# Kernel optimization log

Hardware: AMD Instinct MI355X
Metric: run time of the kernel (lower is better)

The kernel has to match this reference:

```python
import jax, jax.numpy as jnp
from jax import lax
import numpy as np

DN = ('NCHW', 'OIHW', 'NCHW')

def conv2d(x, w, b, stride=1, padding=1):
    out = lax.conv_general_dilated(
        x, w, window_strides=(stride, stride),
        padding=[(padding, padding), (padding, padding)],
        dimension_numbers=DN)
    return out + b[None, :, None, None]

def maxpool2d(x, k=2, s=2):
    return lax.reduce_window(x, -jnp.inf, lax.max,
                             window_dimensions=(1, 1, k, k),
                             window_strides=(1, 1, s, s),
                             padding='VALID')

def setup_inputs() -> dict:
    key = jax.random.key(0)
    ks = jax.random.split(key, 9)
    B = 4096
    x = jax.random.normal(ks[0], (B, 3, 32, 32), dtype=jnp.float32)
    # weights initialized like torch.randn(...) * 0.1, biases zeros
    w1 = jax.random.normal(ks[1], (16, 3, 3, 3), dtype=jnp.float32) * 0.1
    b1 = jnp.zeros((16,), jnp.float32)
    w2 = jax.random.normal(ks[2], (32, 16, 3, 3), dtype=jnp.float32) * 0.1
    b2 = jnp.zeros((32,), jnp.float32)
    w3 = jax.random.normal(ks[3], (64, 32, 3, 3), dtype=jnp.float32) * 0.1
    b3 = jnp.zeros((64,), jnp.float32)
    # fc: Linear(64*4*4, 10); kaiming-uniform-ish init
    fan_in = 64 * 4 * 4
    bound = 1.0 / np.sqrt(fan_in)
    fc_w = jax.random.uniform(ks[4], (10, fan_in), jnp.float32, -bound, bound)
    fc_b = jax.random.uniform(ks[5], (10,), jnp.float32, -bound, bound)
    return {"x": x, "w1": w1, "b1": b1, "w2": w2, "b2": b2,
            "w3": w3, "b3": b3, "fc_w": fc_w, "fc_b": fc_b}

def reference(x, w1, b1, w2, b2, w3, b3, fc_w, fc_b):
    h = maxpool2d(jax.nn.relu(conv2d(x, w1, b1)))   # [B,16,16,16]
    h = maxpool2d(jax.nn.relu(conv2d(h, w2, b2)))   # [B,32,8,8]
    h = maxpool2d(jax.nn.relu(conv2d(h, w3, b3)))   # [B,64,4,4]
    h = h.reshape(h.shape[0], -1)                    # [B,1024]
    # dropout is identity in eval mode
    return h @ fc_w.T + fc_b
```

## Files before the change

kernel.cpp:

```cpp
#include <hip/hip_runtime.h>

typedef float f32x4 __attribute__((ext_vector_type(4)));
typedef float f32x16v __attribute__((ext_vector_type(16)));
typedef __bf16 bf16x4 __attribute__((ext_vector_type(4)));
typedef __bf16 bf16x8 __attribute__((ext_vector_type(8)));

union U4B8 { uint4 u; bf16x8 b; };

#define B2P_OFF 0
#define B3P_OFF 9216
#define C1P_OFF 46080

__global__ __launch_bounds__(256) void pack_weights(
    const float* __restrict__ w1, const float* __restrict__ w2,
    const float* __restrict__ w3, __bf16* __restrict__ wsb) {
  int i = blockIdx.x * 256 + threadIdx.x;
  if (i < 9216) {
    int f = i >> 9, r = i & 511;
    int l = r >> 3, j = r & 7;
    int t = f >> 1, p = f & 1;
    int ky = t / 3, kx = t % 3;
    int oc = l & 31, ic = ((l >> 5) << 3) + j;
    float v = w2[oc * 144 + ic * 9 + ky * 3 + kx];
    __bf16 hi = (__bf16)v;
    wsb[B2P_OFF + i] = p ? (__bf16)(v - (float)hi) : hi;
  } else if (i < 9216 + 36864) {
    int q = i - 9216;
    int f = q >> 9, r = q & 511;
    int l = r >> 3, j = r & 7;
    int t = f >> 3, nt = (f >> 1) & 3, p = f & 1;
    int ky = t / 3, kx = t % 3;
    int oc = nt * 16 + (l & 15), ic = ((l >> 4) << 3) + j;
    float v = w3[oc * 288 + ic * 9 + ky * 3 + kx];
    __bf16 hi = (__bf16)v;
    wsb[B3P_OFF + q] = p ? (__bf16)(v - (float)hi) : hi;
  } else if (i < 9216 + 36864 + 1024) {
    int q = i - (9216 + 36864);
    int f = q >> 9, r = q & 511;
    int l = r >> 3, j = r & 7;
    int oc = l & 15, kg = l >> 4;
    int half = j >> 2, ic = j & 3;
    float v = 0.f;
    if (ic < 3) {
      if (f == 0) {
        if (kg < 3)            v = w1[oc * 27 + ic * 9 + kg * 3 + half];
        else if (half == 0)    v = w1[oc * 27 + ic * 9 + 0 * 3 + 2];
      } else {
        if (half == 0 && kg < 2) v = w1[oc * 27 + ic * 9 + (kg + 1) * 3 + 2];
      }
    }
    wsb[C1P_OFF + q] = (__bf16)v;
  }
}

__global__ __launch_bounds__(256, 4) void cnn_fused(
    const float* __restrict__ x, const __bf16* __restrict__ wsb,
    const float* __restrict__ b1, const float* __restrict__ b2,
    const float* __restrict__ b3,
    const float* __restrict__ fcw, const float* __restrict__ fcb,
    float* __restrict__ out) {
  __shared__ __align__(16) unsigned char smem[25408];
  __bf16* s_img = (__bf16*)smem;
  __bf16* s2b   = (__bf16*)(smem + 9280);
  __bf16* s3b   = (__bf16*)smem;
  float*  h3s   = (float*)(smem + 9280);

  const __bf16* b2p = wsb + B2P_OFF;
  const __bf16* b3p = wsb + B3P_OFF;
  const __bf16* c1p = wsb + C1P_OFF;

  const int tid = threadIdx.x;
  const int img = blockIdx.x;
  const int w = tid >> 6, lane = tid & 63;

  if (tid < 132) {
    int row, col;
    if (tid < 34)       { row = 0;        col = tid; }
    else if (tid < 68)  { row = 33;       col = tid - 34; }
    else if (tid < 100) { row = tid - 67; col = 0; }
    else                { row = tid - 99; col = 33; }
    *(unsigned long long*)&s_img[(row * 34 + col) * 4] = 0ull;
  } else if (tid >= 248 && tid < 252) {
    *(unsigned long long*)&s_img[4624 + (tid - 248) * 4] = 0ull;
  }
  {
    const float* xg = x + img * 3072;
    const int r = tid * 4;
    const int y = r >> 5, xx = r & 31;
    const f32x4 c0 = *(const f32x4*)&xg[r];
    const f32x4 c1 = *(const f32x4*)&xg[r + 1024];
    const f32x4 c2 = *(const f32x4*)&xg[r + 2048];
    #pragma unroll
    for (int k = 0; k < 4; ++k) {
      bf16x4 pk;
      pk.x = (__bf16)c0[k];
      pk.y = (__bf16)c1[k];
      pk.z = (__bf16)c2[k];
      pk.w = (__bf16)0.f;
      *(bf16x4*)&s_img[((y + 1) * 34 + (xx + k + 1)) * 4] = pk;
    }
  }
  const bf16x8 B1h = *(const bf16x8*)(c1p + lane * 8);
  const bf16x8 B2h = *(const bf16x8*)(c1p + 512 + lane * 8);
  __syncthreads();

  float pooled[16];
  {
    const int xm = lane & 15, kg = lane >> 4;
    const int d1r = (kg == 3) ? 0 : kg;
    const int d1c = (kg == 3) ? 2 : 0;
    const int d2r = (kg == 0) ? 1 : 2;
    const int dd1 = d1r * 34 + d1c;
    const int dd2 = d2r * 34 + 2;
    #pragma unroll
    for (int p = 0; p < 4; ++p) {
      f32x4 acc[2][2];
      #pragma unroll
      for (int ys = 0; ys < 2; ++ys)
        #pragma unroll
        for (int xh = 0; xh < 2; ++xh)
          #pragma unroll
          for (int r = 0; r < 4; ++r) acc[ys][xh][r] = 0.f;
      #pragma unroll
      for (int ys = 0; ys < 2; ++ys) {
        const int yqg = w * 8 + p * 2 + ys;
        #pragma unroll
        for (int xh = 0; xh < 2; ++xh) {
          const int cb = yqg * 34 + xh * 16 + xm;
          const uint2 p0 = *(const uint2*)&s_img[(cb + dd1) * 4];
          const uint2 p1 = *(const uint2*)&s_img[(cb + dd1 + 1) * 4];
          const uint2 p2 = *(const uint2*)&s_img[(cb + dd2) * 4];
          const uint2 p3 = *(const uint2*)&s_img[(cb + dd2 + 1) * 4];
          U4B8 A1, A2;
          A1.u.x = p0.x; A1.u.y = p0.y; A1.u.z = p1.x; A1.u.w = p1.y;
          A2.u.x = p2.x; A2.u.y = p2.y; A2.u.z = p3.x; A2.u.w = p3.y;
          acc[ys][xh] = __builtin_amdgcn_mfma_f32_16x16x32_bf16(A1.b, B1h, acc[ys][xh], 0, 0, 0);
          acc[ys][xh] = __builtin_amdgcn_mfma_f32_16x16x32_bf16(A2.b, B2h, acc[ys][xh], 0, 0, 0);
        }
      }
      #pragma unroll
      for (int xh = 0; xh < 2; ++xh)
        #pragma unroll
        for (int xp2 = 0; xp2 < 2; ++xp2) {
          const float v0 = fmaxf(acc[0][xh][xp2 * 2], acc[0][xh][xp2 * 2 + 1]);
          const float v1 = fmaxf(acc[1][xh][xp2 * 2], acc[1][xh][xp2 * 2 + 1]);
          pooled[p * 4 + xh * 2 + xp2] = fmaxf(v0, v1);
        }
    }
  }

  if (tid < 68) {
    int row, col;
    if (tid < 18)      { row = 0;       col = tid; }
    else if (tid < 36) { row = 17;      col = tid - 18; }
    else if (tid < 52) { row = tid - 35; col = 0; }
    else               { row = tid - 51; col = 17; }
    unsigned long long* p = (unsigned long long*)&s2b[row * 448 + col * 24];
    p[0] = 0ull; p[1] = 0ull; p[2] = 0ull; p[3] = 0ull;
  }
  {
    const int oc = lane & 15, quad = lane >> 4;
    const float bias = b1[oc];
    #pragma unroll
    for (int p = 0; p < 4; ++p)
      #pragma unroll
      for (int xh = 0; xh < 2; ++xh)
        #pragma unroll
        for (int xp2 = 0; xp2 < 2; ++xp2) {
          const float v = fmaxf(pooled[p * 4 + xh * 2 + xp2] + bias, 0.f);
          const int py = w * 4 + p, px = xh * 8 + quad * 2 + xp2;
          s2b[(py + 1) * 448 + (px + 1) * 24 + oc] = (__bf16)v;
        }
  }
  bf16x8 Bf[9];
  #pragma unroll
  for (int t = 0; t < 9; ++t)
    Bf[t] = *(const bf16x8*)(b2p + (t * 2) * 512 + lane * 8);
  __syncthreads();

  float pooled2[8];
  {
    const unsigned short* s2 = (const unsigned short*)s2b;
    const int xm = lane & 15, yoff = (lane >> 4) & 1, kh = lane >> 5;
    #pragma unroll
    for (int i2 = 0; i2 < 2; ++i2) {
      f32x16v acc;
      #pragma unroll
      for (int r = 0; r < 16; ++r) acc[r] = 0.f;
      const int rbase = (4 * w + yoff + 2 * i2) * 448;
      #pragma unroll
      for (int t = 0; t < 9; ++t) {
        const int ky = t / 3, kx = t % 3;
        const int ro = rbase + ky * 448 + (xm + kx) * 24 + kh * 8;
        bf16x8 ah = *(const bf16x8*)&s2[ro];
        acc = __builtin_amdgcn_mfma_f32_32x32x16_bf16(ah, Bf[t], acc, 0, 0, 0);
      }
      #pragma unroll
      for (int bq = 0; bq < 2; ++bq)
        #pragma unroll
        for (int rq = 0; rq < 2; ++rq) {
          const int r0 = bq * 4 + rq * 2;
          pooled2[i2 * 4 + bq * 2 + rq] =
              fmaxf(fmaxf(acc[r0], acc[r0 + 1]), fmaxf(acc[r0 + 8], acc[r0 + 9]));
        }
    }
  }

  if (tid < 36) {
    int row, col;
    if (tid < 10)      { row = 0;       col = tid; }
    else if (tid < 20) { row = 9;       col = tid - 10; }
    else if (tid < 28) { row = tid - 19; col = 0; }
    else               { row = tid - 27; col = 9; }
    unsigned long long* p = (unsigned long long*)&s3b[row * 448 + col * 40];
    #pragma unroll
    for (int u = 0; u < 8; ++u) p[u] = 0ull;
  }
  {
    const int oc = lane & 31, hh = lane >> 5;
    const float bias = b2[oc];
    #pragma unroll
    for (int i2 = 0; i2 < 2; ++i2)
      #pragma unroll
      for (int bq = 0; bq < 2; ++bq)
        #pragma unroll
        for (int rq = 0; rq < 2; ++rq) {
          const float v = fmaxf(pooled2[i2 * 4 + bq * 2 + rq] + bias, 0.f);
          const int py = 2 * w + i2, px = 2 * hh + 4 * bq + rq;
          s3b[(py + 1) * 448 + (px + 1) * 40 + oc] = (__bf16)v;
        }
  }
  __syncthreads();

  {
    const unsigned short* s3 = (const unsigned short*)s3b;
    const int nt = w;
    bf16x8 Bt[9];
    #pragma unroll
    for (int t = 0; t < 9; ++t)
      Bt[t] = *(const bf16x8*)(b3p + (t * 8 + nt * 2) * 512 + lane * 8);
    const int m = lane & 15, quad = lane >> 4;
    const int xm = m & 7, yoff = m >> 3;
    f32x4 acc[4];
    #pragma unroll
    for (int mt = 0; mt < 4; ++mt)
      #pragma unroll
      for (int r = 0; r < 4; ++r) acc[mt][r] = 0.f;
    #pragma unroll
    for (int t = 0; t < 9; ++t) {
      const int ky = t / 3, kx = t % 3;
      #pragma unroll
      for (int mt = 0; mt < 4; ++mt) {
        const int ro = (2 * mt + yoff + ky) * 448 + (xm + kx) * 40 + quad * 8;
        bf16x8 ah = *(const bf16x8*)&s3[ro];
        acc[mt] = __builtin_amdgcn_mfma_f32_16x16x32_bf16(ah, Bt[t], acc[mt], 0, 0, 0);
      }
    }
    const int ocl = lane & 15;
    #pragma unroll
    for (int mt = 0; mt < 4; ++mt) {
      float p0 = fmaxf(acc[mt][0], acc[mt][1]);
      float p1 = fmaxf(acc[mt][2], acc[mt][3]);
      p0 = fmaxf(p0, __shfl_xor(p0, 32, 64));
      p1 = fmaxf(p1, __shfl_xor(p1, 32, 64));
      if (quad < 2) {
        const int oc = nt * 16 + ocl;
        const float bias = b3[oc];
        const int base = oc * 20 + mt * 4 + (quad & 1) * 2;
        h3s[base]     = fmaxf(p0 + bias, 0.f);
        h3s[base + 1] = fmaxf(p1 + bias, 0.f);
      }
    }
  }
  __syncthreads();

  {
    f32x4 hv[4];
    #pragma unroll
    for (int k = 0; k < 4; ++k) hv[k] = *(const f32x4*)&h3s[lane * 20 + k * 4];
    for (int j = w; j < 10; j += 4) {
      const f32x4* fw4 = (const f32x4*)&fcw[j * 1024 + lane * 16];
      float dot = 0.f;
      #pragma unroll
      for (int k = 0; k < 4; ++k) {
        const f32x4 fv = fw4[k];
        dot = fmaf(hv[k][0], fv[0], dot);
        dot = fmaf(hv[k][1], fv[1], dot);
        dot = fmaf(hv[k][2], fv[2], dot);
        dot = fmaf(hv[k][3], fv[3], dot);
      }
      #pragma unroll
      for (int s = 32; s > 0; s >>= 1) dot += __shfl_xor(dot, s, 64);
      if (lane == 0) out[img * 10 + j] = dot + fcb[j];
    }
  }
}

extern "C" void kernel_launch(void* const* d_in, const int* in_sizes, int n_in,
                              void* d_out, int out_size, void* d_ws, size_t ws_size,
                              hipStream_t stream) {
  const float* x   = (const float*)d_in[0];
  const float* w1  = (const float*)d_in[1];
  const float* b1  = (const float*)d_in[2];
  const float* w2  = (const float*)d_in[3];
  const float* b2  = (const float*)d_in[4];
  const float* w3  = (const float*)d_in[5];
  const float* b3  = (const float*)d_in[6];
  const float* fcw = (const float*)d_in[7];
  const float* fcb = (const float*)d_in[8];
  __bf16* wsb = (__bf16*)d_ws;
  float* out = (float*)d_out;

  hipLaunchKernelGGL(pack_weights, dim3(184), dim3(256), 0, stream, w1, w2, w3, wsb);
  hipLaunchKernelGGL(cnn_fused, dim3(4096), dim3(256), 0, stream,
                     x, wsb, b1, b2, b3, fcw, fcb, out);
}
```

Measured before the change: 125.3 us.

## Process two images per workgroup to amortize weight loads and interleave MFMAs

Each 256-thread block now handles two images instead of one, with doubled shared memory (two image buffers) and half the grid. Weight fragments loaded into registers for each conv stage and the FC weights are reused across both images, and independent MFMA chains for the two images are interleaved to hide latency. In exchange register pressure and LDS use double, and the occupancy hint drops from 4 to 3 blocks per CU.

```diff
diff --git a/kernel.cpp b/kernel.cpp
--- a/kernel.cpp
+++ b/kernel.cpp
@@ -53,58 +53,63 @@
   }
 }
 
-__global__ __launch_bounds__(256, 4) void cnn_fused(
+__global__ __launch_bounds__(256, 3) void cnn_fused(
     const float* __restrict__ x, const __bf16* __restrict__ wsb,
     const float* __restrict__ b1, const float* __restrict__ b2,
     const float* __restrict__ b3,
     const float* __restrict__ fcw, const float* __restrict__ fcb,
     float* __restrict__ out) {
-  __shared__ __align__(16) unsigned char smem[25408];
-  __bf16* s_img = (__bf16*)smem;
-  __bf16* s2b   = (__bf16*)(smem + 9280);
-  __bf16* s3b   = (__bf16*)smem;
-  float*  h3s   = (float*)(smem + 9280);
+  __shared__ __align__(16) unsigned char smem[50816];
 
   const __bf16* b2p = wsb + B2P_OFF;
   const __bf16* b3p = wsb + B3P_OFF;
   const __bf16* c1p = wsb + C1P_OFF;
 
   const int tid = threadIdx.x;
-  const int img = blockIdx.x;
   const int w = tid >> 6, lane = tid & 63;
-
-  if (tid < 132) {
-    int row, col;
-    if (tid < 34)       { row = 0;        col = tid; }
-    else if (tid < 68)  { row = 33;       col = tid - 34; }
-    else if (tid < 100) { row = tid - 67; col = 0; }
-    else                { row = tid - 99; col = 33; }
-    *(unsigned long long*)&s_img[(row * 34 + col) * 4] = 0ull;
-  } else if (tid >= 248 && tid < 252) {
-    *(unsigned long long*)&s_img[4624 + (tid - 248) * 4] = 0ull;
-  }
-  {
-    const float* xg = x + img * 3072;
+  const int img0 = blockIdx.x * 2;
+
+  #pragma unroll
+  for (int im = 0; im < 2; ++im) {
+    __bf16* s_img = (__bf16*)(smem + im * 25408);
+    if (tid < 132) {
+      int row, col;
+      if (tid < 34)       { row = 0;        col = tid; }
+      else if (tid < 68)  { row = 33;       col = tid - 34; }
+      else if (tid < 100) { row = tid - 67; col = 0; }
+      else                { row = tid - 99; col = 33; }
+      *(unsigned long long*)&s_img[(row * 34 + col) * 4] = 0ull;
+    } else if (tid >= 248 && tid < 252) {
+      *(unsigned long long*)&s_img[4624 + (tid - 248) * 4] = 0ull;
+    }
+  }
+  {
     const int r = tid * 4;
     const int y = r >> 5, xx = r & 31;
-    const f32x4 c0 = *(const f32x4*)&xg[r];
-    const f32x4 c1 = *(const f32x4*)&xg[r + 1024];
-    const f32x4 c2 = *(const f32x4*)&xg[r + 2048];
+    const float* xg0 = x + img0 * 3072;
+    const float* xg1 = xg0 + 3072;
+    const f32x4 a0 = *(const f32x4*)&xg0[r];
+    const f32x4 a1 = *(const f32x4*)&xg0[r + 1024];
+    const f32x4 a2 = *(const f32x4*)&xg0[r + 2048];
+    const f32x4 d0 = *(const f32x4*)&xg1[r];
+    const f32x4 d1 = *(const f32x4*)&xg1[r + 1024];
+    const f32x4 d2 = *(const f32x4*)&xg1[r + 2048];
+    __bf16* si0 = (__bf16*)smem;
+    __bf16* si1 = (__bf16*)(smem + 25408);
     #pragma unroll
     for (int k = 0; k < 4; ++k) {
-      bf16x4 pk;
-      pk.x = (__bf16)c0[k];
-      pk.y = (__bf16)c1[k];
-      pk.z = (__bf16)c2[k];
-      pk.w = (__bf16)0.f;
-      *(bf16x4*)&s_img[((y + 1) * 34 + (xx + k + 1)) * 4] = pk;
+      bf16x4 pa, pb;
+      pa.x = (__bf16)a0[k]; pa.y = (__bf16)a1[k]; pa.z = (__bf16)a2[k]; pa.w = (__bf16)0.f;
+      pb.x = (__bf16)d0[k]; pb.y = (__bf16)d1[k]; pb.z = (__bf16)d2[k]; pb.w = (__bf16)0.f;
+      *(bf16x4*)&si0[((y + 1) * 34 + (xx + k + 1)) * 4] = pa;
+      *(bf16x4*)&si1[((y + 1) * 34 + (xx + k + 1)) * 4] = pb;
     }
   }
   const bf16x8 B1h = *(const bf16x8*)(c1p + lane * 8);
   const bf16x8 B2h = *(const bf16x8*)(c1p + 512 + lane * 8);
   __syncthreads();
 
-  float pooled[16];
+  float pooled[2][16];
   {
     const int xm = lane & 15, kg = lane >> 4;
     const int d1r = (kg == 3) ? 0 : kg;
@@ -114,63 +119,79 @@
     const int dd2 = d2r * 34 + 2;
     #pragma unroll
     for (int p = 0; p < 4; ++p) {
-      f32x4 acc[2][2];
-      #pragma unroll
-      for (int ys = 0; ys < 2; ++ys)
-        #pragma unroll
-        for (int xh = 0; xh < 2; ++xh)
-          #pragma unroll
-          for (int r = 0; r < 4; ++r) acc[ys][xh][r] = 0.f;
+      f32x4 acc[2][2][2];
+      #pragma unroll
+      for (int im = 0; im < 2; ++im)
+        #pragma unroll
+        for (int ys = 0; ys < 2; ++ys)
+          #pragma unroll
+          for (int xh = 0; xh < 2; ++xh)
+            #pragma unroll
+            for (int r = 0; r < 4; ++r) acc[im][ys][xh][r] = 0.f;
       #pragma unroll
       for (int ys = 0; ys < 2; ++ys) {
         const int yqg = w * 8 + p * 2 + ys;
         #pragma unroll
         for (int xh = 0; xh < 2; ++xh) {
           const int cb = yqg * 34 + xh * 16 + xm;
-          const uint2 p0 = *(const uint2*)&s_img[(cb + dd1) * 4];
-          const uint2 p1 = *(const uint2*)&s_img[(cb + dd1 + 1) * 4];
-          const uint2 p2 = *(const uint2*)&s_img[(cb + dd2) * 4];
-          const uint2 p3 = *(const uint2*)&s_img[(cb + dd2 + 1) * 4];
-          U4B8 A1, A2;
-          A1.u.x = p0.x; A1.u.y = p0.y; A1.u.z = p1.x; A1.u.w = p1.y;
-          A2.u.x = p2.x; A2.u.y = p2.y; A2.u.z = p3.x; A2.u.w = p3.y;
-          acc[ys][xh] = __builtin_amdgcn_mfma_f32_16x16x32_bf16(A1.b, B1h, acc[ys][xh], 0, 0, 0);
-          acc[ys][xh] = __builtin_amdgcn_mfma_f32_16x16x32_bf16(A2.b, B2h, acc[ys][xh], 0, 0, 0);
+          #pragma unroll
+          for (int im = 0; im < 2; ++im) {
+            const __bf16* si = (const __bf16*)(smem + im * 25408);
+            const uint2 p0 = *(const uint2*)&si[(cb + dd1) * 4];
+            const uint2 p1 = *(const uint2*)&si[(cb + dd1 + 1) * 4];
+            const uint2 p2 = *(const uint2*)&si[(cb + dd2) * 4];
+            const uint2 p3 = *(const uint2*)&si[(cb + dd2 + 1) * 4];
+            U4B8 A1, A2;
+            A1.u.x = p0.x; A1.u.y = p0.y; A1.u.z = p1.x; A1.u.w = p1.y;
+            A2.u.x = p2.x; A2.u.y = p2.y; A2.u.z = p3.x; A2.u.w = p3.y;
+            acc[im][ys][xh] = __builtin_amdgcn_mfma_f32_16x16x32_bf16(A1.b, B1h, acc[im][ys][xh], 0, 0, 0);
+            acc[im][ys][xh] = __builtin_amdgcn_mfma_f32_16x16x32_bf16(A2.b, B2h, acc[im][ys][xh], 0, 0, 0);
+          }
         }
       }
       #pragma unroll
-      for (int xh = 0; xh < 2; ++xh)
-        #pragma unroll
-        for (int xp2 = 0; xp2 < 2; ++xp2) {
-          const float v0 = fmaxf(acc[0][xh][xp2 * 2], acc[0][xh][xp2 * 2 + 1]);
-          const float v1 = fmaxf(acc[1][xh][xp2 * 2], acc[1][xh][xp2 * 2 + 1]);
-          pooled[p * 4 + xh * 2 + xp2] = fmaxf(v0, v1);
-        }
-    }
-  }
-
-  if (tid < 68) {
-    int row, col;
-    if (tid < 18)      { row = 0;       col = tid; }
-    else if (tid < 36) { row = 17;      col = tid - 18; }
-    else if (tid < 52) { row = tid - 35; col = 0; }
-    else               { row = tid - 51; col = 17; }
-    unsigned long long* p = (unsigned long long*)&s2b[row * 448 + col * 24];
-    p[0] = 0ull; p[1] = 0ull; p[2] = 0ull; p[3] = 0ull;
+      for (int im = 0; im < 2; ++im)
+        #pragma unroll
+        for (int xh = 0; xh < 2; ++xh)
+          #pragma unroll
+          for (int xp2 = 0; xp2 < 2; ++xp2) {
+            const float v0 = fmaxf(acc[im][0][xh][xp2 * 2], acc[im][0][xh][xp2 * 2 + 1]);
+            const float v1 = fmaxf(acc[im][1][xh][xp2 * 2], acc[im][1][xh][xp2 * 2 + 1]);
+            pooled[im][p * 4 + xh * 2 + xp2] = fmaxf(v0, v1);
+          }
+    }
+  }
+
+  #pragma unroll
+  for (int im = 0; im < 2; ++im) {
+    __bf16* s2b = (__bf16*)(smem + im * 25408 + 9280);
+    if (tid < 68) {
+      int row, col;
+      if (tid < 18)      { row = 0;       col = tid; }
+      else if (tid < 36) { row = 17;      col = tid - 18; }
+      else if (tid < 52) { row = tid - 35; col = 0; }
+      else               { row = tid - 51; col = 17; }
+      unsigned long long* p = (unsigned long long*)&s2b[row * 448 + col * 24];
+      p[0] = 0ull; p[1] = 0ull; p[2] = 0ull; p[3] = 0ull;
+    }
   }
   {
     const int oc = lane & 15, quad = lane >> 4;
     const float bias = b1[oc];
     #pragma unroll
-    for (int p = 0; p < 4; ++p)
-      #pragma unroll
-      for (int xh = 0; xh < 2; ++xh)
-        #pragma unroll
-        for (int xp2 = 0; xp2 < 2; ++xp2) {
-          const float v = fmaxf(pooled[p * 4 + xh * 2 + xp2] + bias, 0.f);
-          const int py = w * 4 + p, px = xh * 8 + quad * 2 + xp2;
-          s2b[(py + 1) * 448 + (px + 1) * 24 + oc] = (__bf16)v;
-        }
+    for (int im = 0; im < 2; ++im) {
+      __bf16* s2b = (__bf16*)(smem + im * 25408 + 9280);
+      #pragma unroll
+      for (int p = 0; p < 4; ++p)
+        #pragma unroll
+        for (int xh = 0; xh < 2; ++xh)
+          #pragma unroll
+          for (int xp2 = 0; xp2 < 2; ++xp2) {
+            const float v = fmaxf(pooled[im][p * 4 + xh * 2 + xp2] + bias, 0.f);
+            const int py = w * 4 + p, px = xh * 8 + quad * 2 + xp2;
+            s2b[(py + 1) * 448 + (px + 1) * 24 + oc] = (__bf16)v;
+          }
+    }
   }
   bf16x8 Bf[9];
   #pragma unroll
@@ -178,62 +199,76 @@
     Bf[t] = *(const bf16x8*)(b2p + (t * 2) * 512 + lane * 8);
   __syncthreads();
 
-  float pooled2[8];
-  {
-    const unsigned short* s2 = (const unsigned short*)s2b;
+  float pooled2[2][8];
+  {
+    const unsigned short* s2_0 = (const unsigned short*)(smem + 9280);
+    const unsigned short* s2_1 = (const unsigned short*)(smem + 25408 + 9280);
     const int xm = lane & 15, yoff = (lane >> 4) & 1, kh = lane >> 5;
     #pragma unroll
     for (int i2 = 0; i2 < 2; ++i2) {
-      f32x16v acc;
-      #pragma unroll
-      for (int r = 0; r < 16; ++r) acc[r] = 0.f;
+      f32x16v accA, accB;
+      #pragma unroll
+      for (int r = 0; r < 16; ++r) { accA[r] = 0.f; accB[r] = 0.f; }
       const int rbase = (4 * w + yoff + 2 * i2) * 448;
       #pragma unroll
       for (int t = 0; t < 9; ++t) {
         const int ky = t / 3, kx = t % 3;
         const int ro = rbase + ky * 448 + (xm + kx) * 24 + kh * 8;
-        bf16x8 ah = *(const bf16x8*)&s2[ro];
-        acc = __builtin_amdgcn_mfma_f32_32x32x16_bf16(ah, Bf[t], acc, 0, 0, 0);
+        bf16x8 a0 = *(const bf16x8*)&s2_0[ro];
+        bf16x8 a1 = *(const bf16x8*)&s2_1[ro];
+        accA = __builtin_amdgcn_mfma_f32_32x32x16_bf16(a0, Bf[t], accA, 0, 0, 0);
+        accB = __builtin_amdgcn_mfma_f32_32x32x16_bf16(a1, Bf[t], accB, 0, 0, 0);
       }
       #pragma unroll
       for (int bq = 0; bq < 2; ++bq)
         #pragma unroll
         for (int rq = 0; rq < 2; ++rq) {
           const int r0 = bq * 4 + rq * 2;
-          pooled2[i2 * 4 + bq * 2 + rq] =
-              fmaxf(fmaxf(acc[r0], acc[r0 + 1]), fmaxf(acc[r0 + 8], acc[r0 + 9]));
+          pooled2[0][i2 * 4 + bq * 2 + rq] =
+              fmaxf(fmaxf(accA[r0], accA[r0 + 1]), fmaxf(accA[r0 + 8], accA[r0 + 9]));
+          pooled2[1][i2 * 4 + bq * 2 + rq] =
+              fmaxf(fmaxf(accB[r0], accB[r0 + 1]), fmaxf(accB[r0 + 8], accB[r0 + 9]));
         }
     }
   }
 
-  if (tid < 36) {
-    int row, col;
-    if (tid < 10)      { row = 0;       col = tid; }
-    else if (tid < 20) { row = 9;       col = tid - 10; }
-    else if (tid < 28) { row = tid - 19; col = 0; }
-    else               { row = tid - 27; col = 9; }
-    unsigned long long* p = (unsigned long long*)&s3b[row * 448 + col * 40];
-    #pragma unroll
-    for (int u = 0; u < 8; ++u) p[u] = 0ull;
+  #pragma unroll
+  for (int im = 0; im < 2; ++im) {
+    __bf16* s3b = (__bf16*)(smem + im * 25408);
+    if (tid < 36) {
+      int row, col;
+      if (tid < 10)      { row = 0;       col = tid; }
+      else if (tid < 20) { row = 9;       col = tid - 10; }
+      else if (tid < 28) { row = tid - 19; col = 0; }
+      else               { row = tid - 27; col = 9; }
+      unsigned long long* p = (unsigned long long*)&s3b[row * 448 + col * 40];
+      #pragma unroll
+      for (int u = 0; u < 8; ++u) p[u] = 0ull;
+    }
   }
   {
     const int oc = lane & 31, hh = lane >> 5;
     const float bias = b2[oc];
     #pragma unroll
-    for (int i2 = 0; i2 < 2; ++i2)
-      #pragma unroll
-      for (int bq = 0; bq < 2; ++bq)
-        #pragma unroll
-        for (int rq = 0; rq < 2; ++rq) {
-          const float v = fmaxf(pooled2[i2 * 4 + bq * 2 + rq] + bias, 0.f);
-          const int py = 2 * w + i2, px = 2 * hh + 4 * bq + rq;
-          s3b[(py + 1) * 448 + (px + 1) * 40 + oc] = (__bf16)v;
-        }
+    for (int im = 0; im < 2; ++im) {
+      __bf16* s3b = (__bf16*)(smem + im * 25408);
+      #pragma unroll
+      for (int i2 = 0; i2 < 2; ++i2)
+        #pragma unroll
+        for (int bq = 0; bq < 2; ++bq)
+          #pragma unroll
+          for (int rq = 0; rq < 2; ++rq) {
+            const float v = fmaxf(pooled2[im][i2 * 4 + bq * 2 + rq] + bias, 0.f);
+            const int py = 2 * w + i2, px = 2 * hh + 4 * bq + rq;
+            s3b[(py + 1) * 448 + (px + 1) * 40 + oc] = (__bf16)v;
+          }
+    }
   }
   __syncthreads();
 
   {
-    const unsigned short* s3 = (const unsigned short*)s3b;
+    const unsigned short* s3_0 = (const unsigned short*)smem;
+    const unsigned short* s3_1 = (const unsigned short*)(smem + 25408);
     const int nt = w;
     bf16x8 Bt[9];
     #pragma unroll
@@ -241,57 +276,80 @@
       Bt[t] = *(const bf16x8*)(b3p + (t * 8 + nt * 2) * 512 + lane * 8);
     const int m = lane & 15, quad = lane >> 4;
     const int xm = m & 7, yoff = m >> 3;
-    f32x4 acc[4];
-    #pragma unroll
-    for (int mt = 0; mt < 4; ++mt)
-      #pragma unroll
-      for (int r = 0; r < 4; ++r) acc[mt][r] = 0.f;
+    f32x4 acc[2][4];
+    #pragma unroll
+    for (int im = 0; im < 2; ++im)
+      #pragma unroll
+      for (int mt = 0; mt < 4; ++mt)
+        #pragma unroll
+        for (int r = 0; r < 4; ++r) acc[im][mt][r] = 0.f;
     #pragma unroll
     for (int t = 0; t < 9; ++t) {
       const int ky = t / 3, kx = t % 3;
       #pragma unroll
       for (int mt = 0; mt < 4; ++mt) {
         const int ro = (2 * mt + yoff + ky) * 448 + (xm + kx) * 40 + quad * 8;
-        bf16x8 ah = *(const bf16x8*)&s3[ro];
-        acc[mt] = __builtin_amdgcn_mfma_f32_16x16x32_bf16(ah, Bt[t], acc[mt], 0, 0, 0);
+        bf16x8 a0 = *(const bf16x8*)&s3_0[ro];
+        bf16x8 a1 = *(const bf16x8*)&s3_1[ro];
+        acc[0][mt] = __builtin_amdgcn_mfma_f32_16x16x32_bf16(a0, Bt[t], acc[0][mt], 0, 0, 0);
+        acc[1][mt] = __builtin_amdgcn_mfma_f32_16x16x32_bf16(a1, Bt[t], acc[1][mt], 0, 0, 0);
       }
     }
     const int ocl = lane & 15;
     #pragma unroll
-    for (int mt = 0; mt < 4; ++mt) {
-      float p0 = fmaxf(acc[mt][0], acc[mt][1]);
-      float p1 = fmaxf(acc[mt][2], acc[mt][3]);
-      p0 = fmaxf(p0, __shfl_xor(p0, 32, 64));
-      p1 = fmaxf(p1, __shfl_xor(p1, 32, 64));
-      if (quad < 2) {
-        const int oc = nt * 16 + ocl;
-        const float bias = b3[oc];
-        const int base = oc * 20 + mt * 4 + (quad & 1) * 2;
-        h3s[base]     = fmaxf(p0 + bias, 0.f);
-        h3s[base + 1] = fmaxf(p1 + bias, 0.f);
+    for (int im = 0; im < 2; ++im) {
+      float* h3s = (float*)(smem + im * 25408 + 9280);
+      #pragma unroll
+      for (int mt = 0; mt < 4; ++mt) {
+        float p0 = fmaxf(acc[im][mt][0], acc[im][mt][1]);
+        float p1 = fmaxf(acc[im][mt][2], acc[im][mt][3]);
+        p0 = fmaxf(p0, __shfl_xor(p0, 32, 64));
+        p1 = fmaxf(p1, __shfl_xor(p1, 32, 64));
+        if (quad < 2) {
+          const int oc = nt * 16 + ocl;
+          const float bias = b3[oc];
+          const int base = oc * 20 + mt * 4 + (quad & 1) * 2;
+          h3s[base]     = fmaxf(p0 + bias, 0.f);
+          h3s[base + 1] = fmaxf(p1 + bias, 0.f);
+        }
       }
     }
   }
   __syncthreads();
 
   {
-    f32x4 hv[4];
-    #pragma unroll
-    for (int k = 0; k < 4; ++k) hv[k] = *(const f32x4*)&h3s[lane * 20 + k * 4];
+    const float* h3s0 = (const float*)(smem + 9280);
+    const float* h3s1 = (const float*)(smem + 25408 + 9280);
+    f32x4 hvA[4], hvB[4];
+    #pragma unroll
+    for (int k = 0; k < 4; ++k) {
+      hvA[k] = *(const f32x4*)&h3s0[lane * 20 + k * 4];
+      hvB[k] = *(const f32x4*)&h3s1[lane * 20 + k * 4];
+    }
     for (int j = w; j < 10; j += 4) {
       const f32x4* fw4 = (const f32x4*)&fcw[j * 1024 + lane * 16];
-      float dot = 0.f;
+      float dotA = 0.f, dotB = 0.f;
       #pragma unroll
       for (int k = 0; k < 4; ++k) {
         const f32x4 fv = fw4[k];
-        dot = fmaf(hv[k][0], fv[0], dot);
-        dot = fmaf(hv[k][1], fv[1], dot);
-        dot = fmaf(hv[k][2], fv[2], dot);
-        dot = fmaf(hv[k][3], fv[3], dot);
-      }
-      #pragma unroll
-      for (int s = 32; s > 0; s >>= 1) dot += __shfl_xor(dot, s, 64);
-      if (lane == 0) out[img * 10 + j] = dot + fcb[j];
+        dotA = fmaf(hvA[k][0], fv[0], dotA);
+        dotA = fmaf(hvA[k][1], fv[1], dotA);
+        dotA = fmaf(hvA[k][2], fv[2], dotA);
+        dotA = fmaf(hvA[k][3], fv[3], dotA);
+        dotB = fmaf(hvB[k][0], fv[0], dotB);
+        dotB = fmaf(hvB[k][1], fv[1], dotB);
+        dotB = fmaf(hvB[k][2], fv[2], dotB);
+        dotB = fmaf(hvB[k][3], fv[3], dotB);
+      }
+      #pragma unroll
+      for (int s = 32; s > 0; s >>= 1) {
+        dotA += __shfl_xor(dotA, s, 64);
+        dotB += __shfl_xor(dotB, s, 64);
+      }
+      if (lane == 0) {
+        out[img0 * 10 + j]       = dotA + fcb[j];
+        out[(img0 + 1) * 10 + j] = dotB + fcb[j];
+      }
     }
   }
 }
@@ -312,6 +370,6 @@
   float* out = (float*)d_out;
 
   hipLaunchKernelGGL(pack_weights, dim3(184), dim3(256), 0, stream, w1, w2, w3, wsb);
-  hipLaunchKernelGGL(cnn_fused, dim3(4096), dim3(256), 0, stream,
+  hipLaunchKernelGGL(cnn_fused, dim3(2048), dim3(256), 0, stream,
                      x, wsb, b1, b2, b3, fcw, fcb, out);
 }
```

Result: no change. 125.7 us (+0.3%).
